# Kernel tuning notes

Measured on AMD Instinct MI355X. Metric: run time of the kernel, lower is better.

The kernel has to match this reference:

```python
import jax, jax.numpy as jnp
import numpy as np

TAU = 0.1          # temperature from init_kwargs
EPS = 1e-8         # torch.nn.CosineSimilarity default eps


def setup_inputs() -> dict:
    key = jax.random.key(0)
    k1, k2, k3 = jax.random.split(key, 3)
    B, D = 2048, 128
    return {
        "z_i": jax.random.normal(k1, (B, D), dtype=jnp.float32),
        "z_j": jax.random.normal(k2, (B, D), dtype=jnp.float32),
        "y": jax.random.randint(k3, (B,), 0, 10, dtype=jnp.int64),
    }


def reference(z_i, z_j, y):
    # p: (2N, D)
    p = jnp.concatenate([z_i, z_j], axis=0)
    n2 = p.shape[0]
    # Cosine similarity via norms + single GEMM (same math as pairwise
    # CosineSimilarity: dot / max(||a||*||b||, eps)), then temperature scale.
    norms = jnp.linalg.norm(p, axis=1)                      # (2N,)
    sim = (p @ p.T) / jnp.maximum(norms[:, None] * norms[None, :], EPS) / TAU

    # Positive mask: same label, diagonal removed.
    y2 = jnp.concatenate([y, y], axis=0)                    # (2N,)
    off_diag = 1.0 - jnp.eye(n2, dtype=sim.dtype)           # logit mask
    mask = (y2[:, None] == y2[None, :]).astype(sim.dtype) * off_diag

    # Masked log-softmax over each row (self excluded from denominator).
    exp_logits = jnp.exp(sim) * off_diag
    log_prob = sim - jnp.log(exp_logits.sum(axis=1, keepdims=True))

    mean_log_prob_pos = (mask * log_prob).sum(axis=1) / mask.sum(axis=1)
    return -mean_log_prob_pos.mean()
```

## Files before the change

### kernel.cpp

```cpp
#include <hip/hip_runtime.h>

#define N2 4096
#define D 128
#define TAU_INV 10.0f
#define JSL 4
#define TPW (N2 / (JSL * 128))
#define GEMM_BLOCKS (128 * JSL)
#define NCLS 10
#define CGRP 16
#define CROWS (N2 / CGRP)
#define CB (NCLS * CGRP)

typedef __attribute__((ext_vector_type(8))) short bf16x8;
typedef __attribute__((ext_vector_type(16))) float floatx16;

__device__ __forceinline__ short f2bf(float f) {
    unsigned u = __float_as_uint(f);
    u = (u + 0x7fff + ((u >> 16) & 1)) >> 16;
    return (short)u;
}
__device__ __forceinline__ float bf2f(short s) {
    return __uint_as_float(((unsigned)(unsigned short)s) << 16);
}

__global__ __launch_bounds__(64) void prep_kernel(const float* __restrict__ zi,
                                                  const float* __restrict__ zj,
                                                  short* __restrict__ qb,
                                                  float* __restrict__ se_g,
                                                  float* __restrict__ S) {
    int row = blockIdx.x;
    int lane = threadIdx.x;
    const float* src = (row < 2048) ? (zi + row * D) : (zj + (row - 2048) * D);
    float2 v = ((const float2*)src)[lane];
    float ss = v.x * v.x + v.y * v.y;
    #pragma unroll
    for (int m = 1; m < 64; m <<= 1) ss += __shfl_xor(ss, m);
    float inv = 1.0f / sqrtf(ss);
    short2 o;
    o.x = f2bf(v.x * inv);
    o.y = f2bf(v.y * inv);
    ((short2*)(qb + row * D))[lane] = o;
    if (lane == 0) se_g[row] = 0.f;
    if (row == 0)
        for (int k = lane; k < NCLS * D + 2 * NCLS; k += 64) S[k] = 0.f;
}

__global__ __launch_bounds__(256) void main_kernel(const short* __restrict__ qb,
                                                   const long long* __restrict__ y,
                                                   float* __restrict__ se_g,
                                                   float* __restrict__ S) {
    int tid = threadIdx.x;

    if (blockIdx.x >= GEMM_BLOCKS) {
        int cb = blockIdx.x - GEMM_BLOCKS;
        int c  = cb / CGRP;
        int g  = cb % CGRP;
        int d  = tid & 127;
        int rh = tid >> 7;
        int r0 = g * CROWS + rh * (CROWS / 2);

        float sS = 0.f, sT = 0.f, cnt = 0.f;
        #pragma unroll 4
        for (int i = 0; i < CROWS / 2; ++i) {
            int r = r0 + i;
            bool m = ((int)y[r & 2047] == c);
            float q = bf2f(qb[r * D + d]);
            sS += m ? q : 0.f;
            sT += m ? q * q : 0.f;
            cnt += m ? 1.f : 0.f;
        }

        __shared__ float shS[256];
        __shared__ float shT[4];
        __shared__ float shC[2];
        shS[tid] = sS;
        #pragma unroll
        for (int m = 1; m < 64; m <<= 1) sT += __shfl_xor(sT, m);
        if ((tid & 63) == 0) shT[tid >> 6] = sT;
        if (d == 0) shC[rh] = cnt;
        __syncthreads();
        if (tid < 128) atomicAdd(&S[c * D + tid], shS[tid] + shS[tid + 128]);
        if (tid == 0) {
            atomicAdd(&S[NCLS * D + c], shT[0] + shT[1] + shT[2] + shT[3]);
            atomicAdd(&S[NCLS * D + NCLS + c], shC[0] + shC[1]);
        }
        return;
    }

    int wave = tid >> 6;
    int lane = tid & 63;
    int col  = lane & 31;
    int half = lane >> 5;
    int it = blockIdx.x >> 2;
    int js = blockIdx.x & (JSL - 1);
    int i0 = it * 32;
    int jbase = js * (N2 / JSL);

    const short* ap = qb + (i0 + col) * D + half * 8;
    bf16x8 af[8];
    #pragma unroll
    for (int k = 0; k < 8; ++k) af[k] = *(const bf16x8*)(ap + k * 16);

    float se[16];
    #pragma unroll
    for (int r = 0; r < 16; ++r) se[r] = 0.f;

    bf16x8 bf[8];
    {
        const short* bp = qb + (jbase + wave * 32 + col) * D + half * 8;
        #pragma unroll
        for (int k = 0; k < 8; ++k) bf[k] = *(const bf16x8*)(bp + k * 16);
    }

    #pragma unroll
    for (int t = 0; t < TPW; ++t) {
        int j0 = jbase + (wave + 4 * t) * 32;

        bf16x8 bn[8];
        if (t < TPW - 1) {
            const short* bp = qb + (j0 + 128 + col) * D + half * 8;
            #pragma unroll
            for (int k = 0; k < 8; ++k) bn[k] = *(const bf16x8*)(bp + k * 16);
        }

        floatx16 acc;
        #pragma unroll
        for (int r = 0; r < 16; ++r) acc[r] = 0.f;
        #pragma unroll
        for (int k = 0; k < 8; ++k)
            acc = __builtin_amdgcn_mfma_f32_32x32x16_bf16(af[k], bf[k], acc, 0, 0, 0);

        if (j0 == i0) {
            int jcol = j0 + col;
            #pragma unroll
            for (int r = 0; r < 16; ++r) {
                int rowr = i0 + (r & 3) + 8 * (r >> 2) + 4 * half;
                float e = __expf(acc[r] * TAU_INV);
                se[r] += (rowr == jcol) ? 0.f : e;
            }
        } else {
            #pragma unroll
            for (int r = 0; r < 16; ++r)
                se[r] += __expf(acc[r] * TAU_INV);
        }

        if (t < TPW - 1) {
            #pragma unroll
            for (int k = 0; k < 8; ++k) bf[k] = bn[k];
        }
    }

    #pragma unroll
    for (int r = 0; r < 16; ++r) {
        float a = se[r];
        #pragma unroll
        for (int m = 1; m < 32; m <<= 1) a += __shfl_xor(a, m);
        if (col == 0) {
            int rowr = i0 + (r & 3) + 8 * (r >> 2) + 4 * half;
            atomicAdd(&se_g[rowr], a);
        }
    }
}

__global__ __launch_bounds__(256) void finish_kernel(const float* __restrict__ se_g,
                                                     const float* __restrict__ S,
                                                     float* __restrict__ out) {
    int tid = threadIdx.x;
    int wave = tid >> 6;
    int lane = tid & 63;

    float P = 0.f;
    for (int c = wave; c < NCLS; c += 4) {
        float2 sv = ((const float2*)(S + c * D))[lane];
        float s2 = sv.x * sv.x + sv.y * sv.y;
        #pragma unroll
        for (int m = 1; m < 64; m <<= 1) s2 += __shfl_xor(s2, m);
        float n = S[NCLS * D + NCLS + c];
        P += (n >= 2.0f) ? (s2 - S[NCLS * D + c]) * TAU_INV / (n - 1.0f) : 0.f;
    }

    float L = 0.f;
    for (int i = tid; i < N2; i += 256) L += __logf(se_g[i]);
    #pragma unroll
    for (int m = 1; m < 64; m <<= 1) L += __shfl_xor(L, m);

    __shared__ float red[8];
    if (lane == 0) { red[wave] = L; red[4 + wave] = P; }
    __syncthreads();
    if (tid == 0) {
        float Ls = red[0] + red[1] + red[2] + red[3];
        float Ps = red[4] + red[5] + red[6] + red[7];
        out[0] = (Ls - Ps) * (1.0f / (float)N2);
    }
}

extern "C" void kernel_launch(void* const* d_in, const int* in_sizes, int n_in,
                              void* d_out, int out_size, void* d_ws, size_t ws_size,
                              hipStream_t stream) {
    const float*     zi = (const float*)d_in[0];
    const float*     zj = (const float*)d_in[1];
    const long long* y  = (const long long*)d_in[2];
    float* out = (float*)d_out;

    char* ws = (char*)d_ws;
    short* qb   = (short*)ws;
    float* se_g = (float*)(ws + N2 * D * sizeof(short));
    float* S    = se_g + N2;

    prep_kernel<<<N2, 64, 0, stream>>>(zi, zj, qb, se_g, S);
    main_kernel<<<GEMM_BLOCKS + CB, 256, 0, stream>>>(qb, y, se_g, S);
    finish_kernel<<<1, 256, 0, stream>>>(se_g, S, out);
}
```

Measured before the change: 98.55 us.

## Fuse finish into main kernel, add MFMA-tiled layout, double j-split, use exp2

The finish kernel is folded into the main kernel through a last-block-done atomic counter, which removes one launch. The prep kernel now also writes a second copy of the normalized bf16 data in a fragment-ordered layout, so each lane's MFMA operand loads are contiguous. The j-dimension split is doubled to 8, giving twice as many GEMM blocks for occupancy. exp is replaced by exp2 with a prescaled constant, and the explicit register double-buffering of B is dropped. Costs include an extra layout write in prep, more atomics on se_g, and the class-sum blocks are now scheduled first.

Result: slower. 158.5 us (+60.8%).

```diff
diff --git a/kernel.cpp b/kernel.cpp
--- a/kernel.cpp
+++ b/kernel.cpp
@@ -3,13 +3,15 @@
 #define N2 4096
 #define D 128
 #define TAU_INV 10.0f
-#define JSL 4
+#define E2SCALE 14.4269504088896340736f
+#define JSL 8
 #define TPW (N2 / (JSL * 128))
 #define GEMM_BLOCKS (128 * JSL)
 #define NCLS 10
 #define CGRP 16
 #define CROWS (N2 / CGRP)
 #define CB (NCLS * CGRP)
+#define TOTB (CB + GEMM_BLOCKS)
 
 typedef __attribute__((ext_vector_type(8))) short bf16x8;
 typedef __attribute__((ext_vector_type(16))) float floatx16;
@@ -26,8 +28,10 @@
 __global__ __launch_bounds__(64) void prep_kernel(const float* __restrict__ zi,
                                                   const float* __restrict__ zj,
                                                   short* __restrict__ qb,
+                                                  short* __restrict__ qb2,
                                                   float* __restrict__ se_g,
-                                                  float* __restrict__ S) {
+                                                  float* __restrict__ S,
+                                                  unsigned* __restrict__ done) {
     int row = blockIdx.x;
     int lane = threadIdx.x;
     const float* src = (row < 2048) ? (zi + row * D) : (zj + (row - 2048) * D);
@@ -40,19 +44,34 @@
     o.x = f2bf(v.x * inv);
     o.y = f2bf(v.y * inv);
     ((short2*)(qb + row * D))[lane] = o;
+    int addr2 = (row >> 5) * 4096 + (lane >> 2) * 256 + (row & 31) * 8 + 2 * (lane & 3);
+    *(short2*)(qb2 + addr2) = o;
     if (lane == 0) se_g[row] = 0.f;
-    if (row == 0)
+    if (row == 0) {
         for (int k = lane; k < NCLS * D + 2 * NCLS; k += 64) S[k] = 0.f;
+        if (lane == 0) *done = 0u;
+    }
 }
 
 __global__ __launch_bounds__(256) void main_kernel(const short* __restrict__ qb,
+                                                   const short* __restrict__ qb2,
                                                    const long long* __restrict__ y,
                                                    float* __restrict__ se_g,
-                                                   float* __restrict__ S) {
+                                                   float* __restrict__ S,
+                                                   unsigned* __restrict__ done,
+                                                   float* __restrict__ out) {
+    __shared__ float shS[256];
+    __shared__ float shT[4];
+    __shared__ float shC[2];
+    __shared__ float red[8];
+    __shared__ unsigned lastflag;
+
     int tid = threadIdx.x;
-
-    if (blockIdx.x >= GEMM_BLOCKS) {
-        int cb = blockIdx.x - GEMM_BLOCKS;
+    int wave = tid >> 6;
+    int lane = tid & 63;
+
+    if (blockIdx.x < CB) {
+        int cb = blockIdx.x;
         int c  = cb / CGRP;
         int g  = cb % CGRP;
         int d  = tid & 127;
@@ -70,9 +89,6 @@
             cnt += m ? 1.f : 0.f;
         }
 
-        __shared__ float shS[256];
-        __shared__ float shT[4];
-        __shared__ float shC[2];
         shS[tid] = sS;
         #pragma unroll
         for (int m = 1; m < 64; m <<= 1) sT += __shfl_xor(sT, m);
@@ -84,113 +100,94 @@
             atomicAdd(&S[NCLS * D + c], shT[0] + shT[1] + shT[2] + shT[3]);
             atomicAdd(&S[NCLS * D + NCLS + c], shC[0] + shC[1]);
         }
-        return;
+    } else {
+        int gb = blockIdx.x - CB;
+        int col  = lane & 31;
+        int half = lane >> 5;
+        int it = gb >> 3;
+        int js = gb & (JSL - 1);
+        int i0 = it * 32;
+        int jbase = js * (N2 / JSL);
+
+        const short* ap = qb2 + it * 4096 + lane * 8;
+        bf16x8 af[8];
+        #pragma unroll
+        for (int k = 0; k < 8; ++k) af[k] = *(const bf16x8*)(ap + k * 512);
+
+        float se[16];
+        #pragma unroll
+        for (int r = 0; r < 16; ++r) se[r] = 0.f;
+
+        #pragma unroll
+        for (int t = 0; t < TPW; ++t) {
+            int j0 = jbase + (wave + 4 * t) * 32;
+            const short* bp = qb2 + (j0 >> 5) * 4096 + lane * 8;
+            bf16x8 bf[8];
+            #pragma unroll
+            for (int k = 0; k < 8; ++k) bf[k] = *(const bf16x8*)(bp + k * 512);
+
+            floatx16 acc;
+            #pragma unroll
+            for (int r = 0; r < 16; ++r) acc[r] = 0.f;
+            #pragma unroll
+            for (int k = 0; k < 8; ++k)
+                acc = __builtin_amdgcn_mfma_f32_32x32x16_bf16(af[k], bf[k], acc, 0, 0, 0);
+
+            if (j0 == i0) {
+                int jcol = j0 + col;
+                #pragma unroll
+                for (int r = 0; r < 16; ++r) {
+                    int rowr = i0 + (r & 3) + 8 * (r >> 2) + 4 * half;
+                    float e = __builtin_amdgcn_exp2f(acc[r] * E2SCALE);
+                    se[r] += (rowr == jcol) ? 0.f : e;
+                }
+            } else {
+                #pragma unroll
+                for (int r = 0; r < 16; ++r)
+                    se[r] += __builtin_amdgcn_exp2f(acc[r] * E2SCALE);
+            }
+        }
+
+        #pragma unroll
+        for (int r = 0; r < 16; ++r) {
+            float a = se[r];
+            #pragma unroll
+            for (int m = 1; m < 32; m <<= 1) a += __shfl_xor(a, m);
+            if (col == 0) {
+                int rowr = i0 + (r & 3) + 8 * (r >> 2) + 4 * half;
+                atomicAdd(&se_g[rowr], a);
+            }
+        }
     }
 
-    int wave = tid >> 6;
-    int lane = tid & 63;
-    int col  = lane & 31;
-    int half = lane >> 5;
-    int it = blockIdx.x >> 2;
-    int js = blockIdx.x & (JSL - 1);
-    int i0 = it * 32;
-    int jbase = js * (N2 / JSL);
-
-    const short* ap = qb + (i0 + col) * D + half * 8;
-    bf16x8 af[8];
-    #pragma unroll
-    for (int k = 0; k < 8; ++k) af[k] = *(const bf16x8*)(ap + k * 16);
-
-    float se[16];
-    #pragma unroll
-    for (int r = 0; r < 16; ++r) se[r] = 0.f;
-
-    bf16x8 bf[8];
-    {
-        const short* bp = qb + (jbase + wave * 32 + col) * D + half * 8;
-        #pragma unroll
-        for (int k = 0; k < 8; ++k) bf[k] = *(const bf16x8*)(bp + k * 16);
-    }
-
-    #pragma unroll
-    for (int t = 0; t < TPW; ++t) {
-        int j0 = jbase + (wave + 4 * t) * 32;
-
-        bf16x8 bn[8];
-        if (t < TPW - 1) {
-            const short* bp = qb + (j0 + 128 + col) * D + half * 8;
-            #pragma unroll
-            for (int k = 0; k < 8; ++k) bn[k] = *(const bf16x8*)(bp + k * 16);
-        }
-
-        floatx16 acc;
-        #pragma unroll
-        for (int r = 0; r < 16; ++r) acc[r] = 0.f;
-        #pragma unroll
-        for (int k = 0; k < 8; ++k)
-            acc = __builtin_amdgcn_mfma_f32_32x32x16_bf16(af[k], bf[k], acc, 0, 0, 0);
-
-        if (j0 == i0) {
-            int jcol = j0 + col;
-            #pragma unroll
-            for (int r = 0; r < 16; ++r) {
-                int rowr = i0 + (r & 3) + 8 * (r >> 2) + 4 * half;
-                float e = __expf(acc[r] * TAU_INV);
-                se[r] += (rowr == jcol) ? 0.f : e;
-            }
-        } else {
-            #pragma unroll
-            for (int r = 0; r < 16; ++r)
-                se[r] += __expf(acc[r] * TAU_INV);
-        }
-
-        if (t < TPW - 1) {
-            #pragma unroll
-            for (int k = 0; k < 8; ++k) bf[k] = bn[k];
-        }
-    }
-
-    #pragma unroll
-    for (int r = 0; r < 16; ++r) {
-        float a = se[r];
-        #pragma unroll
-        for (int m = 1; m < 32; m <<= 1) a += __shfl_xor(a, m);
-        if (col == 0) {
-            int rowr = i0 + (r & 3) + 8 * (r >> 2) + 4 * half;
-            atomicAdd(&se_g[rowr], a);
-        }
-    }
-}
-
-__global__ __launch_bounds__(256) void finish_kernel(const float* __restrict__ se_g,
-                                                     const float* __restrict__ S,
-                                                     float* __restrict__ out) {
-    int tid = threadIdx.x;
-    int wave = tid >> 6;
-    int lane = tid & 63;
-
-    float P = 0.f;
-    for (int c = wave; c < NCLS; c += 4) {
-        float2 sv = ((const float2*)(S + c * D))[lane];
-        float s2 = sv.x * sv.x + sv.y * sv.y;
-        #pragma unroll
-        for (int m = 1; m < 64; m <<= 1) s2 += __shfl_xor(s2, m);
-        float n = S[NCLS * D + NCLS + c];
-        P += (n >= 2.0f) ? (s2 - S[NCLS * D + c]) * TAU_INV / (n - 1.0f) : 0.f;
-    }
-
-    float L = 0.f;
-    for (int i = tid; i < N2; i += 256) L += __logf(se_g[i]);
-    #pragma unroll
-    for (int m = 1; m < 64; m <<= 1) L += __shfl_xor(L, m);
-
-    __shared__ float red[8];
-    if (lane == 0) { red[wave] = L; red[4 + wave] = P; }
+    __threadfence();
+    if (tid == 0) lastflag = (atomicAdd(done, 1u) == TOTB - 1) ? 1u : 0u;
     __syncthreads();
-    if (tid == 0) {
-        float Ls = red[0] + red[1] + red[2] + red[3];
-        float Ps = red[4] + red[5] + red[6] + red[7];
-        out[0] = (Ls - Ps) * (1.0f / (float)N2);
+    if (lastflag) {
+        __threadfence();
+
+        float P = 0.f;
+        for (int c = wave; c < NCLS; c += 4) {
+            float2 sv = ((const float2*)(S + c * D))[lane];
+            float s2 = sv.x * sv.x + sv.y * sv.y;
+            #pragma unroll
+            for (int m = 1; m < 64; m <<= 1) s2 += __shfl_xor(s2, m);
+            float n = S[NCLS * D + NCLS + c];
+            P += (n >= 2.0f) ? (s2 - S[NCLS * D + c]) * TAU_INV / (n - 1.0f) : 0.f;
+        }
+
+        float L = 0.f;
+        for (int i = tid; i < N2; i += 256) L += __logf(se_g[i]);
+        #pragma unroll
+        for (int m = 1; m < 64; m <<= 1) L += __shfl_xor(L, m);
+
+        if (lane == 0) { red[wave] = L; red[4 + wave] = P; }
+        __syncthreads();
+        if (tid == 0) {
+            float Ls = red[0] + red[1] + red[2] + red[3];
+            float Ps = red[4] + red[5] + red[6] + red[7];
+            out[0] = (Ls - Ps) * (1.0f / (float)N2);
+        }
     }
 }
 
@@ -203,11 +200,12 @@
     float* out = (float*)d_out;
 
     char* ws = (char*)d_ws;
-    short* qb   = (short*)ws;
-    float* se_g = (float*)(ws + N2 * D * sizeof(short));
-    float* S    = se_g + N2;
-
-    prep_kernel<<<N2, 64, 0, stream>>>(zi, zj, qb, se_g, S);
-    main_kernel<<<GEMM_BLOCKS + CB, 256, 0, stream>>>(qb, y, se_g, S);
-    finish_kernel<<<1, 256, 0, stream>>>(se_g, S, out);
-}
+    short*    qb   = (short*)ws;
+    short*    qb2  = qb + N2 * D;
+    float*    se_g = (float*)(ws + 2 * N2 * D * sizeof(short));
+    float*    S    = se_g + N2;
+    unsigned* done = (unsigned*)(S + NCLS * D + 2 * NCLS);
+
+    prep_kernel<<<N2, 64, 0, stream>>>(zi, zj, qb, qb2, se_g, S, done);
+    main_kernel<<<TOTB, 256, 0, stream>>>(qb, qb2, y, se_g, S, done, out);
+}
```
